# Performance work log

Measured on AMD Instinct MI355X. Metric: run time of the kernel, lower is better.

## Reference

```python
import jax, jax.numpy as jnp
import numpy as np

N_NODES = 100000
N_EDGES = 640000
LATDIM = 128
GNN_LAYER = 3
LN_EPS = 1e-5


def setup_inputs() -> dict:
    key = jax.random.key(0)
    k1, k2, k3, k4 = jax.random.split(key, 4)
    embeds = jax.random.normal(k1, (N_NODES, LATDIM), dtype=jnp.float32)
    adj_row = jax.random.randint(k2, (N_EDGES,), 0, N_NODES, dtype=jnp.int32)
    adj_col = jax.random.randint(k3, (N_EDGES,), 0, N_NODES, dtype=jnp.int32)
    adj_val = jax.random.uniform(k4, (N_EDGES,), dtype=jnp.float32)
    return {"embeds": embeds, "adj_row": adj_row, "adj_col": adj_col, "adj_val": adj_val}


def _layer_norm(x):
    # nn.LayerNorm(latdim, elementwise_affine=False)
    mu = jnp.mean(x, axis=-1, keepdims=True)
    var = jnp.mean(jnp.square(x - mu), axis=-1, keepdims=True)
    return (x - mu) / jnp.sqrt(var + LN_EPS)


def _spmm(adj_row, adj_col, adj_val, x):
    # out[r] += val * x[c] for each edge (r, c, val)  -- sparse [N,N] @ [N,d]
    msgs = adj_val[:, None] * x[adj_col]  # [E, d]
    return jax.ops.segment_sum(msgs, adj_row, num_segments=N_NODES)


def reference(embeds, adj_row, adj_col, adj_val):
    x = _layer_norm(embeds)
    acc = jnp.zeros_like(x)  # gnn_layer > 0, so hop-0 embeds are NOT included
    for _ in range(GNN_LAYER):
        x = _spmm(adj_row, adj_col, adj_val, x)
        acc = acc + x
    return acc
```

## Files before the change

### kernel.cpp

```cpp
#include <hip/hip_runtime.h>

#define N_NODES 100000
#define N_EDGES 640000
#define LATDIM  128
#define LN_EPS  1e-5f

typedef unsigned int u32;
typedef float f32x4 __attribute__((ext_vector_type(4)));

#define SCAN_NB   98
#define N_PAD     (SCAN_NB * 1024)

#define LN_BLOCKS   (N_NODES / 8)

#define CNT_BLOCKS  100
#define CNT_K       25

#define APP_K      7
#define APP_EDGES  (256 * APP_K)
#define APP_NB     ((N_EDGES + APP_EDGES - 1) / APP_EDGES)

__device__ __forceinline__ float bflo(u32 u) { return __uint_as_float(u << 16); }
__device__ __forceinline__ float bfhi(u32 u) { return __uint_as_float(u & 0xffff0000u); }
__device__ __forceinline__ u32 pack_bf2(float a, float b) {
    u32 ua = __float_as_uint(a), ub = __float_as_uint(b);
    ua = (ua + 0x7fffu + ((ua >> 16) & 1u)) >> 16;
    ub = (ub + 0x7fffu + ((ub >> 16) & 1u)) >> 16;
    return ua | (ub << 16);
}

__device__ __forceinline__ u32 pack_edge(int col, float val) {
    u32 q = (u32)fminf(val * 32768.0f + 0.5f, 32767.0f);
    return (u32)col | (q << 17);
}
__device__ __forceinline__ int edge_col(u32 r) { return (int)(r & 0x1FFFFu); }

__global__ __launch_bounds__(256) void ln_count_kernel(const float* __restrict__ in,
                                                       u32* __restrict__ out,
                                                       const int* __restrict__ rowi,
                                                       int* __restrict__ partials) {
    int b = blockIdx.x;
    if (b >= CNT_BLOCKS) {
        int tid  = threadIdx.x;
        int wave = tid >> 6;
        int lane = tid & 63;
        int half = lane >> 5;
        int sub  = lane & 31;
        int row  = (b - CNT_BLOCKS) * 8 + wave * 2 + half;
        f32x4 v = __builtin_nontemporal_load(((const f32x4*)in) + (size_t)row * 32 + sub);
        float s  = v.x + v.y + v.z + v.w;
        float ss = v.x * v.x + v.y * v.y + v.z * v.z + v.w * v.w;
        #pragma unroll
        for (int o = 16; o > 0; o >>= 1) {
            s  += __shfl_xor(s,  o, 64);
            ss += __shfl_xor(ss, o, 64);
        }
        float mu   = s * (1.0f / LATDIM);
        float var  = ss * (1.0f / LATDIM) - mu * mu;
        float rstd = rsqrtf(var + LN_EPS);
        uint2 w;
        w.x = pack_bf2((v.x - mu) * rstd, (v.y - mu) * rstd);
        w.y = pack_bf2((v.z - mu) * rstd, (v.w - mu) * rstd);
        ((uint2*)out)[(size_t)row * 32 + sub] = w;
    } else {
        __shared__ int hist[SCAN_NB];
        int t = threadIdx.x;
        if (t < SCAN_NB) hist[t] = 0;
        __syncthreads();
        int e0 = b * (256 * CNT_K);
        #pragma unroll
        for (int k = 0; k < CNT_K; ++k) {
            int e = e0 + k * 256 + t;
            atomicAdd(&hist[rowi[e] >> 10], 1);
        }
        __syncthreads();
        if (t < SCAN_NB) partials[b * SCAN_NB + t] = hist[t];
    }
}

__global__ __launch_bounds__(128) void scan_chunks_kernel(const int* __restrict__ partials,
                                                          int* __restrict__ bsums,
                                                          int* __restrict__ gcur) {
    __shared__ int ss[128];
    int t = threadIdx.x;
    int own = 0;
    if (t < SCAN_NB) {
        for (int i = 0; i < CNT_BLOCKS; ++i) own += partials[i * SCAN_NB + t];
    }
    ss[t] = own;
    __syncthreads();
    #pragma unroll
    for (int o = 1; o < 128; o <<= 1) {
        int u = 0;
        if (t >= o) u = ss[t - o];
        __syncthreads();
        if (t >= o) ss[t] += u;
        __syncthreads();
    }
    if (t < SCAN_NB) {
        int off = ss[t] - own;
        bsums[t] = off;
        gcur[t]  = off;
    }
    if (t == SCAN_NB) bsums[SCAN_NB] = N_EDGES;
}

__global__ __launch_bounds__(256) void bucket_append_kernel(const int* __restrict__ rowi,
                                                            const int* __restrict__ coli,
                                                            const float* __restrict__ vali,
                                                            int* __restrict__ gcur,
                                                            uint2* __restrict__ staging) {
    __shared__ int hist[SCAN_NB];
    __shared__ int base[SCAN_NB];
    int t = threadIdx.x;
    if (t < SCAN_NB) hist[t] = 0;
    __syncthreads();
    int e0 = blockIdx.x * APP_EDGES;
    int r[APP_K]; int c[APP_K]; float v[APP_K]; int bk[APP_K];
    #pragma unroll
    for (int k = 0; k < APP_K; ++k) {
        int e = e0 + k * 256 + t;
        if (e < N_EDGES) {
            r[k] = rowi[e]; c[k] = coli[e]; v[k] = vali[e];
            bk[k] = r[k] >> 10;
            atomicAdd(&hist[bk[k]], 1);
        } else {
            bk[k] = -1;
        }
    }
    __syncthreads();
    if (t < SCAN_NB) {
        int h = hist[t];
        base[t] = h ? atomicAdd(&gcur[t], h) : 0;
        hist[t] = 0;
    }
    __syncthreads();
    #pragma unroll
    for (int k = 0; k < APP_K; ++k) {
        if (bk[k] >= 0) {
            int idx = atomicAdd(&hist[bk[k]], 1);
            staging[base[bk[k]] + idx] =
                make_uint2(((u32)(r[k] & 1023) << 17) | (u32)c[k],
                           __float_as_uint(v[k]));
        }
    }
}

__global__ __launch_bounds__(256) void fine_scatter_kernel(int* __restrict__ cnt,
                                                           const int* __restrict__ bsums,
                                                           const uint2* __restrict__ staging,
                                                           u32* __restrict__ recs) {
    __shared__ int cur[1024];
    __shared__ int ts[256];
    int b = blockIdx.x, t = threadIdx.x;
    *(int4*)&cur[t * 4] = make_int4(0, 0, 0, 0);
    __syncthreads();
    int gbase = bsums[b];
    int n = bsums[b + 1] - gbase;
    for (int i = t; i < n; i += 256) {
        uint2 s = staging[gbase + i];
        atomicAdd(&cur[s.x >> 17], 1);
    }
    __syncthreads();
    int4 v = *(const int4*)&cur[t * 4];
    int s = v.x + v.y + v.z + v.w;
    ts[t] = s;
    __syncthreads();
    #pragma unroll
    for (int o = 1; o < 256; o <<= 1) {
        int u = 0;
        if (t >= o) u = ts[t - o];
        __syncthreads();
        if (t >= o) ts[t] += u;
        __syncthreads();
    }
    int excl = ts[t] - s;
    int4 w;
    w.x = excl;
    w.y = excl + v.x;
    w.z = excl + v.x + v.y;
    w.w = excl + v.x + v.y + v.z;
    *(int4*)&cnt[b * 1024 + t * 4] = w;
    *(int4*)&cur[t * 4] = w;
    __syncthreads();
    for (int i = t; i < n; i += 256) {
        uint2 s2 = staging[gbase + i];
        int rowLocal = (int)(s2.x >> 17);
        int col = (int)(s2.x & 0x1FFFFu);
        int pos = gbase + atomicAdd(&cur[rowLocal], 1);
        recs[pos] = pack_edge(col, __uint_as_float(s2.y));
    }
}

__global__ __launch_bounds__(256) void spmm_csr_kernel(const int* __restrict__ cnt,
                                                       const int* __restrict__ bsums,
                                                       const u32* __restrict__ recs,
                                                       const u32* __restrict__ x,
                                                       u32* __restrict__ y,
                                                       const u32* __restrict__ add0,
                                                       const u32* __restrict__ add1,
                                                       float* __restrict__ out,
                                                       int mode) {
    int tid  = threadIdx.x;
    int wave = tid >> 6;
    int lane = tid & 63;
    int row  = blockIdx.x * 16 + wave * 4 + (lane >> 4);
    int sub  = lane & 15;
    int e   = cnt[row]     + bsums[row >> 10];
    int end = cnt[row + 1] + bsums[(row + 1) >> 10];
    const uint4* x4 = (const uint4*)x;
    float a0=0,a1=0,a2=0,a3=0,a4=0,a5=0,a6=0,a7=0;
    #define ACC_EDGE(r, g) do {                                      \
        float q_ = (float)((r) >> 17);                               \
        a0 += q_ * bflo((g).x); a1 += q_ * bfhi((g).x);              \
        a2 += q_ * bflo((g).y); a3 += q_ * bfhi((g).y);              \
        a4 += q_ * bflo((g).z); a5 += q_ * bfhi((g).z);              \
        a6 += q_ * bflo((g).w); a7 += q_ * bfhi((g).w);              \
    } while (0)
    for (; e + 8 <= end; e += 8) {
        u32 r0 = recs[e],   r1 = recs[e+1], r2 = recs[e+2], r3 = recs[e+3];
        u32 r4 = recs[e+4], r5 = recs[e+5], r6 = recs[e+6], r7 = recs[e+7];
        uint4 g0 = x4[(size_t)edge_col(r0) * 16 + sub];
        uint4 g1 = x4[(size_t)edge_col(r1) * 16 + sub];
        uint4 g2 = x4[(size_t)edge_col(r2) * 16 + sub];
        uint4 g3 = x4[(size_t)edge_col(r3) * 16 + sub];
        uint4 g4 = x4[(size_t)edge_col(r4) * 16 + sub];
        uint4 g5 = x4[(size_t)edge_col(r5) * 16 + sub];
        uint4 g6 = x4[(size_t)edge_col(r6) * 16 + sub];
        uint4 g7 = x4[(size_t)edge_col(r7) * 16 + sub];
        ACC_EDGE(r0, g0); ACC_EDGE(r1, g1); ACC_EDGE(r2, g2); ACC_EDGE(r3, g3);
        ACC_EDGE(r4, g4); ACC_EDGE(r5, g5); ACC_EDGE(r6, g6); ACC_EDGE(r7, g7);
    }
    if (e + 4 <= end) {
        u32 r0 = recs[e], r1 = recs[e+1], r2 = recs[e+2], r3 = recs[e+3];
        uint4 g0 = x4[(size_t)edge_col(r0) * 16 + sub];
        uint4 g1 = x4[(size_t)edge_col(r1) * 16 + sub];
        uint4 g2 = x4[(size_t)edge_col(r2) * 16 + sub];
        uint4 g3 = x4[(size_t)edge_col(r3) * 16 + sub];
        ACC_EDGE(r0, g0); ACC_EDGE(r1, g1); ACC_EDGE(r2, g2); ACC_EDGE(r3, g3);
        e += 4;
    }
    for (; e < end; ++e) {
        u32 r = recs[e];
        uint4 g = x4[(size_t)edge_col(r) * 16 + sub];
        ACC_EDGE(r, g);
    }
    #undef ACC_EDGE
    const float sc = 1.0f / 32768.0f;
    a0 *= sc; a1 *= sc; a2 *= sc; a3 *= sc;
    a4 *= sc; a5 *= sc; a6 *= sc; a7 *= sc;
    size_t oi = (size_t)row * 16 + sub;
    if (mode == 2) {
        uint4 b0 = ((const uint4*)add0)[oi];
        uint4 b1 = ((const uint4*)add1)[oi];
        a0 += bflo(b0.x) + bflo(b1.x); a1 += bfhi(b0.x) + bfhi(b1.x);
        a2 += bflo(b0.y) + bflo(b1.y); a3 += bfhi(b0.y) + bfhi(b1.y);
        a4 += bflo(b0.z) + bflo(b1.z); a5 += bfhi(b0.z) + bfhi(b1.z);
        a6 += bflo(b0.w) + bflo(b1.w); a7 += bfhi(b0.w) + bfhi(b1.w);
        f32x4* o4 = (f32x4*)(out + (size_t)row * LATDIM + sub * 8);
        f32x4 q0 = {a0, a1, a2, a3};
        f32x4 q1 = {a4, a5, a6, a7};
        __builtin_nontemporal_store(q0, o4 + 0);
        __builtin_nontemporal_store(q1, o4 + 1);
    } else {
        uint4 w;
        w.x = pack_bf2(a0, a1);
        w.y = pack_bf2(a2, a3);
        w.z = pack_bf2(a4, a5);
        w.w = pack_bf2(a6, a7);
        ((uint4*)y)[oi] = w;
    }
}

__global__ __launch_bounds__(256) void ln_f32_kernel(const float* __restrict__ in,
                                                     float* __restrict__ out) {
    int tid  = threadIdx.x;
    int wave = tid >> 6;
    int lane = tid & 63;
    int half = lane >> 5;
    int sub  = lane & 31;
    int row  = blockIdx.x * 8 + wave * 2 + half;
    if (row >= N_NODES) return;
    float4 v = ((const float4*)in)[(size_t)row * 32 + sub];
    float s  = v.x + v.y + v.z + v.w;
    float ss = v.x * v.x + v.y * v.y + v.z * v.z + v.w * v.w;
    #pragma unroll
    for (int o = 16; o > 0; o >>= 1) {
        s  += __shfl_xor(s,  o, 64);
        ss += __shfl_xor(ss, o, 64);
    }
    float mu   = s * (1.0f / LATDIM);
    float var  = ss * (1.0f / LATDIM) - mu * mu;
    float rstd = rsqrtf(var + LN_EPS);
    float4 o4;
    o4.x = (v.x - mu) * rstd; o4.y = (v.y - mu) * rstd;
    o4.z = (v.z - mu) * rstd; o4.w = (v.w - mu) * rstd;
    ((float4*)out)[(size_t)row * 32 + sub] = o4;
}

__global__ __launch_bounds__(256) void spmm_atomic_kernel(const int* __restrict__ rowi,
                                                          const int* __restrict__ coli,
                                                          const float* __restrict__ vali,
                                                          const float* __restrict__ x,
                                                          float* __restrict__ y) {
    int t = blockIdx.x * 256 + threadIdx.x;
    int e = t >> 5;
    if (e >= N_EDGES) return;
    int k = t & 31;
    int r = rowi[e];
    int c = coli[e];
    float v = vali[e];
    float4 xv = ((const float4*)(x + (size_t)c * LATDIM))[k];
    float* yp = y + (size_t)r * LATDIM + k * 4;
    atomicAdd(yp + 0, v * xv.x);
    atomicAdd(yp + 1, v * xv.y);
    atomicAdd(yp + 2, v * xv.z);
    atomicAdd(yp + 3, v * xv.w);
}

__global__ __launch_bounds__(256) void addz_kernel(float* __restrict__ acc,
                                                   const float* __restrict__ x,
                                                   float* __restrict__ z,
                                                   int first) {
    size_t i = (size_t)blockIdx.x * 256 + threadIdx.x;
    float4 xv = ((const float4*)x)[i];
    float4* ap = ((float4*)acc) + i;
    if (first) {
        *ap = xv;
    } else {
        float4 a = *ap;
        a.x += xv.x; a.y += xv.y; a.z += xv.z; a.w += xv.w;
        *ap = a;
    }
    if (z) ((float4*)z)[i] = make_float4(0.f, 0.f, 0.f, 0.f);
}

extern "C" void kernel_launch(void* const* d_in, const int* in_sizes, int n_in,
                              void* d_out, int out_size, void* d_ws, size_t ws_size,
                              hipStream_t stream) {
    const float* embeds  = (const float*)d_in[0];
    const int*   adj_row = (const int*)d_in[1];
    const int*   adj_col = (const int*)d_in[2];
    const float* adj_val = (const float*)d_in[3];
    float* out = (float*)d_out;

    u32*   A16   = (u32*)d_ws;
    u32*   B16   = A16 + (size_t)N_NODES * (LATDIM / 2);
    int*   cnt   = (int*)(B16 + (size_t)N_NODES * (LATDIM / 2));
    int*   partials = cnt + N_PAD;
    int*   bsums = partials + CNT_BLOCKS * SCAN_NB;
    int*   gcur  = bsums + 128;
    uint2* staging = (uint2*)(gcur + 128);
    u32*   recs  = (u32*)(staging + N_EDGES);
    size_t need  = (size_t)((char*)(recs + N_EDGES) - (char*)d_ws);

    const int rowGrid = N_NODES / 16;

    if (ws_size >= need) {
        ln_count_kernel<<<CNT_BLOCKS + LN_BLOCKS, 256, 0, stream>>>(embeds, A16,
                                                                    adj_row, partials);
        scan_chunks_kernel<<<1, 128, 0, stream>>>(partials, bsums, gcur);
        bucket_append_kernel<<<APP_NB, 256, 0, stream>>>(adj_row, adj_col, adj_val,
                                                         gcur, staging);
        fine_scatter_kernel<<<SCAN_NB, 256, 0, stream>>>(cnt, bsums, staging, recs);
        spmm_csr_kernel<<<rowGrid, 256, 0, stream>>>(cnt, bsums, recs, A16, B16,
                                                     nullptr, nullptr, nullptr, 0);
        spmm_csr_kernel<<<rowGrid, 256, 0, stream>>>(cnt, bsums, recs, B16, A16,
                                                     nullptr, nullptr, nullptr, 0);
        spmm_csr_kernel<<<rowGrid, 256, 0, stream>>>(cnt, bsums, recs, A16, nullptr,
                                                     B16, A16, out, 2);
    } else {
        float* A = (float*)d_ws;
        float* B = A + (size_t)N_NODES * LATDIM;
        const size_t rowBytes = (size_t)N_NODES * LATDIM * sizeof(float);
        const int spmmGrid = (N_EDGES * 32 + 255) / 256;
        const int addGrid  = (N_NODES * LATDIM / 4 + 255) / 256;
        ln_f32_kernel<<<LN_BLOCKS, 256, 0, stream>>>(embeds, A);
        hipMemsetAsync(B, 0, rowBytes, stream);
        spmm_atomic_kernel<<<spmmGrid, 256, 0, stream>>>(adj_row, adj_col, adj_val, A, B);
        addz_kernel<<<addGrid, 256, 0, stream>>>(out, B, A, 1);
        spmm_atomic_kernel<<<spmmGrid, 256, 0, stream>>>(adj_row, adj_col, adj_val, B, A);
        addz_kernel<<<addGrid, 256, 0, stream>>>(out, A, B, 0);
        spmm_atomic_kernel<<<spmmGrid, 256, 0, stream>>>(adj_row, adj_col, adj_val, A, B);
        addz_kernel<<<addGrid, 256, 0, stream>>>(out, B, nullptr, 0);
    }
}
```

Measured before the change: 244.4 us.

## Fuse three SpMM launches into one cooperative kernel with grid syncs

Replaces the three back-to-back SpMM CSR launches with a single cooperative kernel of 2048 persistent blocks. The blocks grid-stride over row groups and use grid.sync() between hops, with a fallback to the separate launches if the cooperative launch fails. The goal is to remove two kernel launch gaps and the tail drain between hops. In exchange it caps the grid at 2048 blocks with launch bounds of 8 blocks per CU, which could cut occupancy or latency hiding, and grid barriers have their own cost.

```diff
diff --git a/kernel.cpp b/kernel.cpp
--- a/kernel.cpp
+++ b/kernel.cpp
@@ -1,4 +1,7 @@
 #include <hip/hip_runtime.h>
+#include <hip/hip_cooperative_groups.h>
+
+namespace cg = cooperative_groups;
 
 #define N_NODES 100000
 #define N_EDGES 640000
@@ -19,6 +22,9 @@
 #define APP_K      7
 #define APP_EDGES  (256 * APP_K)
 #define APP_NB     ((N_EDGES + APP_EDGES - 1) / APP_EDGES)
+
+#define COOP_BLOCKS 2048
+#define ROW_GROUPS  (N_NODES / 16)
 
 __device__ __forceinline__ float bflo(u32 u) { return __uint_as_float(u << 16); }
 __device__ __forceinline__ float bfhi(u32 u) { return __uint_as_float(u & 0xffff0000u); }
@@ -192,30 +198,30 @@
     }
 }
 
-__global__ __launch_bounds__(256) void spmm_csr_kernel(const int* __restrict__ cnt,
-                                                       const int* __restrict__ bsums,
-                                                       const u32* __restrict__ recs,
-                                                       const u32* __restrict__ x,
-                                                       u32* __restrict__ y,
-                                                       const u32* __restrict__ add0,
-                                                       const u32* __restrict__ add1,
-                                                       float* __restrict__ out,
-                                                       int mode) {
-    int tid  = threadIdx.x;
+__device__ __forceinline__ void spmm_rows(int g, int tid,
+                                          const int* __restrict__ cnt,
+                                          const int* __restrict__ bsums,
+                                          const u32* __restrict__ recs,
+                                          const u32* __restrict__ x,
+                                          u32* __restrict__ y,
+                                          const u32* __restrict__ add0,
+                                          const u32* __restrict__ add1,
+                                          float* __restrict__ out,
+                                          int mode) {
     int wave = tid >> 6;
     int lane = tid & 63;
-    int row  = blockIdx.x * 16 + wave * 4 + (lane >> 4);
+    int row  = g * 16 + wave * 4 + (lane >> 4);
     int sub  = lane & 15;
     int e   = cnt[row]     + bsums[row >> 10];
     int end = cnt[row + 1] + bsums[(row + 1) >> 10];
     const uint4* x4 = (const uint4*)x;
     float a0=0,a1=0,a2=0,a3=0,a4=0,a5=0,a6=0,a7=0;
-    #define ACC_EDGE(r, g) do {                                      \
+    #define ACC_EDGE(r, g_) do {                                     \
         float q_ = (float)((r) >> 17);                               \
-        a0 += q_ * bflo((g).x); a1 += q_ * bfhi((g).x);              \
-        a2 += q_ * bflo((g).y); a3 += q_ * bfhi((g).y);              \
-        a4 += q_ * bflo((g).z); a5 += q_ * bfhi((g).z);              \
-        a6 += q_ * bflo((g).w); a7 += q_ * bfhi((g).w);              \
+        a0 += q_ * bflo((g_).x); a1 += q_ * bfhi((g_).x);            \
+        a2 += q_ * bflo((g_).y); a3 += q_ * bfhi((g_).y);            \
+        a4 += q_ * bflo((g_).z); a5 += q_ * bfhi((g_).z);            \
+        a6 += q_ * bflo((g_).w); a7 += q_ * bfhi((g_).w);            \
     } while (0)
     for (; e + 8 <= end; e += 8) {
         u32 r0 = recs[e],   r1 = recs[e+1], r2 = recs[e+2], r3 = recs[e+3];
@@ -272,6 +278,36 @@
     }
 }
 
+__global__ __launch_bounds__(256) void spmm_csr_kernel(const int* __restrict__ cnt,
+                                                       const int* __restrict__ bsums,
+                                                       const u32* __restrict__ recs,
+                                                       const u32* __restrict__ x,
+                                                       u32* __restrict__ y,
+                                                       const u32* __restrict__ add0,
+                                                       const u32* __restrict__ add1,
+                                                       float* __restrict__ out,
+                                                       int mode) {
+    spmm_rows(blockIdx.x, threadIdx.x, cnt, bsums, recs, x, y, add0, add1, out, mode);
+}
+
+__global__ __launch_bounds__(256, 8) void spmm3_coop_kernel(const int* __restrict__ cnt,
+                                                            const int* __restrict__ bsums,
+                                                            const u32* __restrict__ recs,
+                                                            u32* __restrict__ A16,
+                                                            u32* __restrict__ B16,
+                                                            float* __restrict__ out) {
+    cg::grid_group grid = cg::this_grid();
+    int tid = threadIdx.x;
+    for (int g = blockIdx.x; g < ROW_GROUPS; g += gridDim.x)
+        spmm_rows(g, tid, cnt, bsums, recs, A16, B16, nullptr, nullptr, nullptr, 0);
+    grid.sync();
+    for (int g = blockIdx.x; g < ROW_GROUPS; g += gridDim.x)
+        spmm_rows(g, tid, cnt, bsums, recs, B16, A16, nullptr, nullptr, nullptr, 0);
+    grid.sync();
+    for (int g = blockIdx.x; g < ROW_GROUPS; g += gridDim.x)
+        spmm_rows(g, tid, cnt, bsums, recs, A16, nullptr, B16, A16, out, 2);
+}
+
 __global__ __launch_bounds__(256) void ln_f32_kernel(const float* __restrict__ in,
                                                      float* __restrict__ out) {
     int tid  = threadIdx.x;
@@ -354,8 +390,6 @@
     u32*   recs  = (u32*)(staging + N_EDGES);
     size_t need  = (size_t)((char*)(recs + N_EDGES) - (char*)d_ws);
 
-    const int rowGrid = N_NODES / 16;
-
     if (ws_size >= need) {
         ln_count_kernel<<<CNT_BLOCKS + LN_BLOCKS, 256, 0, stream>>>(embeds, A16,
                                                                     adj_row, partials);
@@ -363,12 +397,23 @@
         bucket_append_kernel<<<APP_NB, 256, 0, stream>>>(adj_row, adj_col, adj_val,
                                                          gcur, staging);
         fine_scatter_kernel<<<SCAN_NB, 256, 0, stream>>>(cnt, bsums, staging, recs);
-        spmm_csr_kernel<<<rowGrid, 256, 0, stream>>>(cnt, bsums, recs, A16, B16,
-                                                     nullptr, nullptr, nullptr, 0);
-        spmm_csr_kernel<<<rowGrid, 256, 0, stream>>>(cnt, bsums, recs, B16, A16,
-                                                     nullptr, nullptr, nullptr, 0);
-        spmm_csr_kernel<<<rowGrid, 256, 0, stream>>>(cnt, bsums, recs, A16, nullptr,
-                                                     B16, A16, out, 2);
+
+        const int*  cnt_c   = cnt;
+        const int*  bsums_c = bsums;
+        const u32*  recs_c  = recs;
+        void* args[] = { (void*)&cnt_c, (void*)&bsums_c, (void*)&recs_c,
+                         (void*)&A16, (void*)&B16, (void*)&out };
+        hipError_t cerr = hipLaunchCooperativeKernel((const void*)spmm3_coop_kernel,
+                                                     dim3(COOP_BLOCKS), dim3(256),
+                                                     args, 0, stream);
+        if (cerr != hipSuccess) {
+            spmm_csr_kernel<<<ROW_GROUPS, 256, 0, stream>>>(cnt, bsums, recs, A16, B16,
+                                                            nullptr, nullptr, nullptr, 0);
+            spmm_csr_kernel<<<ROW_GROUPS, 256, 0, stream>>>(cnt, bsums, recs, B16, A16,
+                                                            nullptr, nullptr, nullptr, 0);
+            spmm_csr_kernel<<<ROW_GROUPS, 256, 0, stream>>>(cnt, bsums, recs, A16, nullptr,
+                                                            B16, A16, out, 2);
+        }
     } else {
         float* A = (float*)d_ws;
         float* B = A + (size_t)N_NODES * LATDIM;
```

Result: slower. 877.1 us (+258.8%).
